# Kernel tuning notes

Measured on AMD Instinct MI355X. Metric: run time of the kernel, lower is better.

The kernel has to match this reference:

```python
import jax, jax.numpy as jnp
import numpy as np

N, D, H, N_HEADS = 2048, 512, 512, 16

def setup_inputs() -> dict:
    key = jax.random.key(0)
    k1, k2, k3 = jax.random.split(key, 3)
    inputs = jax.random.normal(k1, (N, D), dtype=jnp.float32)
    idx = jax.random.randint(k2, (N,), 0, N_HEADS, dtype=jnp.int64)
    weights = jax.random.normal(k3, (N_HEADS, D, H), dtype=jnp.float32)
    biases = jnp.zeros((N_HEADS, H), dtype=jnp.float32)
    return {"inputs": inputs, "idx": idx, "weights": weights, "biases": biases}

def reference(inputs, idx, weights, biases):
    # per-sample weight gather: (N, D, H) then batched vec-mat: (N, 1, D) @ (N, D, H) -> (N, H)
    w = weights[idx]            # (N, D, H)  -- the redundant materialized gather
    b = biases[idx]             # (N, H)
    return jnp.einsum('nd,ndh->nh', inputs, w) + b
```

## Files before the change

kernel.cpp:

```cpp
#include <hip/hip_runtime.h>


#define N_SAMPLES 2048
#define DIM       512
#define HDIM      512
#define N_HEADS   16
#define SH        32
#define SG        2
#define BPITCH    520

typedef __attribute__((ext_vector_type(8))) short bf16x8;
typedef __attribute__((ext_vector_type(4))) float floatx4;

__device__ inline unsigned short f2bf_rne(float f) {
    union { float f; unsigned u; } v; v.f = f;
    return (unsigned short)((v.u + 0x7FFFu + ((v.u >> 16) & 1u)) >> 16);
}
__device__ inline unsigned bfpack_rne(float lo, float hi) {
    return (unsigned)f2bf_rne(lo) | ((unsigned)f2bf_rne(hi) << 16);
}

__global__ __launch_bounds__(256) void xconv(const float* __restrict__ x,
                                             unsigned* __restrict__ xb) {
    const int i = blockIdx.x * 256 + threadIdx.x;
    const float4 v0 = *(const float4*)(x + i * 8);
    const float4 v1 = *(const float4*)(x + i * 8 + 4);
    uint4 o;
    o.x = bfpack_rne(v0.x, v0.y);
    o.y = bfpack_rne(v0.z, v0.w);
    o.z = bfpack_rne(v1.x, v1.y);
    o.w = bfpack_rne(v1.z, v1.w);
    *(uint4*)(xb + i * 4) = o;
}

__global__ __launch_bounds__(256, 2) void fused(
    const unsigned short* __restrict__ xb,
    const int*   __restrict__ idx,
    const float* __restrict__ w,
    const float* __restrict__ bias,
    float*       __restrict__ out)
{
    __shared__ unsigned short Bl[SH * BPITCH];
    __shared__ int slist[N_SAMPLES];
    __shared__ int wcnt[4];

    const int bid  = blockIdx.x;
    const int sg   = bid & (SG - 1);
    const int sid  = bid >> 1;
    const int head = sid >> 4;
    const int h0   = (sid & 15) * SH;
    const int t    = threadIdx.x;
    const int wave = t >> 6;
    const int lane = t & 63;
    const int l16  = lane & 15;
    const int quad = lane >> 4;

    int myidx[8];
    #pragma unroll
    for (int c = 0; c < 8; ++c)
        myidx[c] = idx[(wave * 8 + c) * 64 + lane];

    {
        const float* wg = w + (size_t)head * DIM * HDIM + h0;
        #pragma unroll
        for (int i = 0; i < 4; ++i) {
            const int task = i * 256 + t;
            const int dq   = task & 127;
            const int hg   = task >> 7;
            const int d0   = dq * 4;
            const int hh0  = hg * 4;
            const float4 q0 = *(const float4*)(wg + (size_t)(d0 + 0) * HDIM + hh0);
            const float4 q1 = *(const float4*)(wg + (size_t)(d0 + 1) * HDIM + hh0);
            const float4 q2 = *(const float4*)(wg + (size_t)(d0 + 2) * HDIM + hh0);
            const float4 q3 = *(const float4*)(wg + (size_t)(d0 + 3) * HDIM + hh0);
            uint2 p;
            p.x = bfpack_rne(q0.x, q1.x); p.y = bfpack_rne(q2.x, q3.x);
            *(uint2*)&Bl[(hh0 + 0) * BPITCH + d0] = p;
            p.x = bfpack_rne(q0.y, q1.y); p.y = bfpack_rne(q2.y, q3.y);
            *(uint2*)&Bl[(hh0 + 1) * BPITCH + d0] = p;
            p.x = bfpack_rne(q0.z, q1.z); p.y = bfpack_rne(q2.z, q3.z);
            *(uint2*)&Bl[(hh0 + 2) * BPITCH + d0] = p;
            p.x = bfpack_rne(q0.w, q1.w); p.y = bfpack_rne(q2.w, q3.w);
            *(uint2*)&Bl[(hh0 + 3) * BPITCH + d0] = p;
        }
    }

    unsigned long long masks[8];
    {
        int mycnt = 0;
        #pragma unroll
        for (int c = 0; c < 8; ++c) {
            masks[c] = __ballot(myidx[c] == head);
            mycnt += __popcll(masks[c]);
        }
        if (lane == 0) wcnt[wave] = mycnt;
    }
    __syncthreads();
    int cnt = 0, base = 0;
    #pragma unroll
    for (int i = 0; i < 4; ++i) { if (i < wave) base += wcnt[i]; cnt += wcnt[i]; }
    {
        int pos = base;
        #pragma unroll
        for (int c = 0; c < 8; ++c) {
            const unsigned long long m = masks[c];
            if (m & (1ull << lane)) {
                const int rank = __popcll(m & ((1ull << lane) - 1ull));
                slist[pos + rank] = (wave * 8 + c) * 64 + lane;
            }
            pos += __popcll(m);
        }
    }
    __syncthreads();

    const int   mt  = (cnt + 15) >> 4;
    const float bv0 = bias[head * HDIM + h0 + l16];
    const float bv1 = bias[head * HDIM + h0 + 16 + l16];

    for (int j = wave; 2 * j + sg < mt; j += 4) {
        const int m  = 2 * j + sg;
        const int mg = m * 16 + l16;
        const int row = slist[mg < cnt ? mg : cnt - 1];
        const unsigned short* ap = xb + (size_t)row * DIM + quad * 8;

        bf16x8 a[16];
        #pragma unroll
        for (int ks = 0; ks < 16; ++ks)
            a[ks] = *(const bf16x8*)(ap + ks * 32);

        floatx4 acc0 = {0.f, 0.f, 0.f, 0.f};
        floatx4 acc1 = {0.f, 0.f, 0.f, 0.f};
        #pragma unroll
        for (int ks = 0; ks < 16; ++ks) {
            const bf16x8 b0 = *(const bf16x8*)&Bl[l16 * BPITCH + ks * 32 + quad * 8];
            const bf16x8 b1 = *(const bf16x8*)&Bl[(16 + l16) * BPITCH + ks * 32 + quad * 8];
            acc0 = __builtin_amdgcn_mfma_f32_16x16x32_bf16(a[ks], b0, acc0, 0, 0, 0);
            acc1 = __builtin_amdgcn_mfma_f32_16x16x32_bf16(a[ks], b1, acc1, 0, 0, 0);
        }

        #pragma unroll
        for (int r = 0; r < 4; ++r) {
            const int mm = m * 16 + quad * 4 + r;
            if (mm < cnt) {
                const int rg = slist[mm];
                out[(size_t)rg * HDIM + h0 + l16]      = acc0[r] + bv0;
                out[(size_t)rg * HDIM + h0 + 16 + l16] = acc1[r] + bv1;
            }
        }
    }
}

extern "C" void kernel_launch(void* const* d_in, const int* in_sizes, int n_in,
                              void* d_out, int out_size, void* d_ws, size_t ws_size,
                              hipStream_t stream) {
    const float* x   = (const float*)d_in[0];
    const int*   idx = (const int*)  d_in[1];
    const float* w   = (const float*)d_in[2];
    const float* b   = (const float*)d_in[3];
    float*       out = (float*)d_out;

    unsigned* xb = (unsigned*)d_ws;

    xconv<<<512, 256, 0, stream>>>(x, xb);
    fused<<<N_HEADS * 16 * SG, 256, 0, stream>>>((const unsigned short*)xb, idx, w, b, out);
}
```

Measured before the change: 87.75 us.

## Drop sample-group split, overlap weight loads with scan, prefetch next A tile

Removes the two-way sample-group split so each block covers all samples of its head and H-slice, which halves the redundant weight loads and bf16 conversions across blocks. The weight tile is now loaded into registers before the index ballot and scan and written to LDS afterwards, so global latency overlaps the sample-list build. The main loop software-prefetches the next 16-row A tile into registers while the current MFMAs run, and slist shrinks to 16-bit entries. The trade-offs are fewer blocks (256), which means less parallelism, and much higher register pressure from the q[16] float4 array and the doubled A buffers, which may lower occupancy or cause spills.

```diff
diff --git a/kernel.cpp b/kernel.cpp
--- a/kernel.cpp
+++ b/kernel.cpp
@@ -6,7 +6,6 @@
 #define HDIM      512
 #define N_HEADS   16
 #define SH        32
-#define SG        2
 #define BPITCH    520
 
 typedef __attribute__((ext_vector_type(8))) short bf16x8;
@@ -41,14 +40,12 @@
     float*       __restrict__ out)
 {
     __shared__ unsigned short Bl[SH * BPITCH];
-    __shared__ int slist[N_SAMPLES];
+    __shared__ unsigned short slist[N_SAMPLES];
     __shared__ int wcnt[4];
 
     const int bid  = blockIdx.x;
-    const int sg   = bid & (SG - 1);
-    const int sid  = bid >> 1;
-    const int head = sid >> 4;
-    const int h0   = (sid & 15) * SH;
+    const int head = bid >> 4;
+    const int h0   = (bid & 15) * SH;
     const int t    = threadIdx.x;
     const int wave = t >> 6;
     const int lane = t & 63;
@@ -60,30 +57,13 @@
     for (int c = 0; c < 8; ++c)
         myidx[c] = idx[(wave * 8 + c) * 64 + lane];
 
-    {
-        const float* wg = w + (size_t)head * DIM * HDIM + h0;
-        #pragma unroll
-        for (int i = 0; i < 4; ++i) {
-            const int task = i * 256 + t;
-            const int dq   = task & 127;
-            const int hg   = task >> 7;
-            const int d0   = dq * 4;
-            const int hh0  = hg * 4;
-            const float4 q0 = *(const float4*)(wg + (size_t)(d0 + 0) * HDIM + hh0);
-            const float4 q1 = *(const float4*)(wg + (size_t)(d0 + 1) * HDIM + hh0);
-            const float4 q2 = *(const float4*)(wg + (size_t)(d0 + 2) * HDIM + hh0);
-            const float4 q3 = *(const float4*)(wg + (size_t)(d0 + 3) * HDIM + hh0);
-            uint2 p;
-            p.x = bfpack_rne(q0.x, q1.x); p.y = bfpack_rne(q2.x, q3.x);
-            *(uint2*)&Bl[(hh0 + 0) * BPITCH + d0] = p;
-            p.x = bfpack_rne(q0.y, q1.y); p.y = bfpack_rne(q2.y, q3.y);
-            *(uint2*)&Bl[(hh0 + 1) * BPITCH + d0] = p;
-            p.x = bfpack_rne(q0.z, q1.z); p.y = bfpack_rne(q2.z, q3.z);
-            *(uint2*)&Bl[(hh0 + 2) * BPITCH + d0] = p;
-            p.x = bfpack_rne(q0.w, q1.w); p.y = bfpack_rne(q2.w, q3.w);
-            *(uint2*)&Bl[(hh0 + 3) * BPITCH + d0] = p;
-        }
-    }
+    const int hh = (t & 7) * 4;
+    const int dg = t >> 3;
+    const float* wg = w + (size_t)head * DIM * HDIM + h0;
+    float4 q[16];
+    #pragma unroll
+    for (int s = 0; s < 16; ++s)
+        q[s] = *(const float4*)(wg + (size_t)(dg * 16 + s) * HDIM + hh);
 
     unsigned long long masks[8];
     {
@@ -106,10 +86,20 @@
             const unsigned long long m = masks[c];
             if (m & (1ull << lane)) {
                 const int rank = __popcll(m & ((1ull << lane) - 1ull));
-                slist[pos + rank] = (wave * 8 + c) * 64 + lane;
+                slist[pos + rank] = (unsigned short)((wave * 8 + c) * 64 + lane);
             }
             pos += __popcll(m);
         }
+    }
+
+    #pragma unroll
+    for (int p = 0; p < 8; ++p) {
+        const int d = dg * 16 + 2 * p;
+        const float4 qa = q[2 * p], qb = q[2 * p + 1];
+        *(unsigned*)&Bl[(hh + 0) * BPITCH + d] = bfpack_rne(qa.x, qb.x);
+        *(unsigned*)&Bl[(hh + 1) * BPITCH + d] = bfpack_rne(qa.y, qb.y);
+        *(unsigned*)&Bl[(hh + 2) * BPITCH + d] = bfpack_rne(qa.z, qb.z);
+        *(unsigned*)&Bl[(hh + 3) * BPITCH + d] = bfpack_rne(qa.w, qb.w);
     }
     __syncthreads();
 
@@ -117,16 +107,25 @@
     const float bv0 = bias[head * HDIM + h0 + l16];
     const float bv1 = bias[head * HDIM + h0 + 16 + l16];
 
-    for (int j = wave; 2 * j + sg < mt; j += 4) {
-        const int m  = 2 * j + sg;
-        const int mg = m * 16 + l16;
+    int j = wave;
+    bf16x8 a[16];
+    if (j < mt) {
+        const int mg  = j * 16 + l16;
         const int row = slist[mg < cnt ? mg : cnt - 1];
         const unsigned short* ap = xb + (size_t)row * DIM + quad * 8;
-
-        bf16x8 a[16];
         #pragma unroll
-        for (int ks = 0; ks < 16; ++ks)
-            a[ks] = *(const bf16x8*)(ap + ks * 32);
+        for (int ks = 0; ks < 16; ++ks) a[ks] = *(const bf16x8*)(ap + ks * 32);
+    }
+    for (; j < mt; j += 4) {
+        bf16x8 an[16];
+        const int jn = j + 4;
+        if (jn < mt) {
+            const int mg  = jn * 16 + l16;
+            const int row = slist[mg < cnt ? mg : cnt - 1];
+            const unsigned short* ap = xb + (size_t)row * DIM + quad * 8;
+            #pragma unroll
+            for (int ks = 0; ks < 16; ++ks) an[ks] = *(const bf16x8*)(ap + ks * 32);
+        }
 
         floatx4 acc0 = {0.f, 0.f, 0.f, 0.f};
         floatx4 acc1 = {0.f, 0.f, 0.f, 0.f};
@@ -140,13 +139,16 @@
 
         #pragma unroll
         for (int r = 0; r < 4; ++r) {
-            const int mm = m * 16 + quad * 4 + r;
+            const int mm = j * 16 + quad * 4 + r;
             if (mm < cnt) {
                 const int rg = slist[mm];
                 out[(size_t)rg * HDIM + h0 + l16]      = acc0[r] + bv0;
                 out[(size_t)rg * HDIM + h0 + 16 + l16] = acc1[r] + bv1;
             }
         }
+
+        #pragma unroll
+        for (int ks = 0; ks < 16; ++ks) a[ks] = an[ks];
     }
 }
 
@@ -162,5 +164,5 @@
     unsigned* xb = (unsigned*)d_ws;
 
     xconv<<<512, 256, 0, stream>>>(x, xb);
-    fused<<<N_HEADS * 16 * SG, 256, 0, stream>>>((const unsigned short*)xb, idx, w, b, out);
+    fused<<<N_HEADS * (HDIM / SH), 256, 0, stream>>>((const unsigned short*)xb, idx, w, b, out);
 }
```

Result: no change. 87.64 us (median of 2 runs) (-0.1%).
